# Optimization experiments

Hardware: AMD Instinct MI355X
Metric: run time of the kernel (lower is better)

Reference implementation:

```python
import jax, jax.numpy as jnp
import numpy as np

NUM_CLASSES = 2
THRESHOLD = 0.35
NEGPOS_RATIO = 7
VARIANCES = (0.1, 0.2)
B, P, O = 64, 16800, 64  # batch, num_priors, num_objs per image


def point_form(pr):
    # cxcywh -> xyxy
    return jnp.concatenate([pr[:, :2] - pr[:, 2:] / 2, pr[:, :2] + pr[:, 2:] / 2], axis=1)


def jaccard(a, b):
    # a: [A,4] xyxy, b: [Bx,4] xyxy -> IoU [A,Bx]
    lt = jnp.maximum(a[:, None, :2], b[None, :, :2])
    rb = jnp.minimum(a[:, None, 2:], b[None, :, 2:])
    wh = jnp.clip(rb - lt, 0.0)
    inter = wh[..., 0] * wh[..., 1]
    area_a = ((a[:, 2] - a[:, 0]) * (a[:, 3] - a[:, 1]))[:, None]
    area_b = ((b[:, 2] - b[:, 0]) * (b[:, 3] - b[:, 1]))[None, :]
    return inter / (area_a + area_b - inter)


def encode(matched, priors):
    # matched xyxy [P,4], priors cxcywh [P,4]
    g_cxcy = (matched[:, :2] + matched[:, 2:]) / 2 - priors[:, :2]
    g_cxcy = g_cxcy / (VARIANCES[0] * priors[:, 2:])
    g_wh = (matched[:, 2:] - matched[:, :2]) / priors[:, 2:]
    g_wh = jnp.log(g_wh) / VARIANCES[1]
    return jnp.concatenate([g_cxcy, g_wh], axis=1)


def encode_landm(matched, priors):
    # matched [P,10] -> [P,5,2]
    m = matched.reshape(-1, 5, 2)
    g = (m - priors[:, None, :2]) / (VARIANCES[0] * priors[:, None, 2:])
    return g.reshape(-1, 10)


def match_one(truths, labels, landms, priors):
    # truths [O,4], labels [O], landms [O,10]
    overlaps = jaccard(truths, point_form(priors))  # [O,P]
    best_prior_overlap = overlaps.max(axis=1)       # per-gt best IoU
    best_prior_idx = overlaps.argmax(axis=1)
    valid_gt = best_prior_overlap >= 0.2
    best_truth_overlap = overlaps.max(axis=0)       # per-prior best IoU
    best_truth_idx = overlaps.argmax(axis=0)
    # index_fill(2) only for valid gts (best_prior_idx_filter)
    bto = best_truth_overlap.at[best_prior_idx].set(
        jnp.where(valid_gt, 2.0, best_truth_overlap[best_prior_idx]))
    # ensure every gt keeps its best prior
    bti = best_truth_idx.at[best_prior_idx].set(jnp.arange(truths.shape[0]))
    matches = truths[bti]                  # [P,4]
    conf = labels[bti]                     # [P]
    conf = jnp.where(bto < THRESHOLD, 0.0, conf)
    loc = encode(matches, priors)
    landm = encode_landm(landms[bti], priors)
    return loc, conf, landm


def smooth_l1_sum(x, mask):
    ax = jnp.abs(x)
    v = jnp.where(ax < 1.0, 0.5 * ax * ax, ax - 0.5)
    return (v * mask).sum()


def setup_inputs() -> dict:
    key = jax.random.key(0)
    k1, k2, k3, k4, k5, k6, k7, k8 = jax.random.split(key, 8)
    loc_data = jax.random.normal(k1, (B, P, 4), jnp.float32)
    conf_data = jax.random.normal(k2, (B, P, NUM_CLASSES), jnp.float32)
    landm_data = jax.random.normal(k3, (B, P, 10), jnp.float32)
    # priors: cx,cy in (0,1), w,h in (0.02,0.22)
    cxy = jax.random.uniform(k4, (P, 2), jnp.float32)
    wh = jax.random.uniform(k5, (P, 2), jnp.float32) * 0.2 + 0.02
    priors = jnp.concatenate([cxy, wh], axis=1)
    # targets: valid corner boxes + landmarks + label in {1,-1}
    xy1 = jax.random.uniform(k6, (B, O, 2), jnp.float32) * 0.6
    bwh = jax.random.uniform(k7, (B, O, 2), jnp.float32) * 0.3 + 0.05
    boxes = jnp.concatenate([xy1, xy1 + bwh], axis=-1)
    lms = jax.random.uniform(k8, (B, O, 10), jnp.float32)
    lab = jnp.where(jax.random.uniform(jax.random.fold_in(key, 9), (B, O, 1)) < 0.3, -1.0, 1.0)
    targets = jnp.concatenate([boxes, lms, lab], axis=-1)
    return {"loc_data": loc_data, "conf_data": conf_data, "landm_data": landm_data,
            "priors": priors, "targets": targets}


def reference(loc_data, conf_data, landm_data, priors, targets):
    num = loc_data.shape[0]
    num_priors = priors.shape[0]
    truths = targets[:, :, :4]
    landms = targets[:, :, 4:14]
    labels = targets[:, :, -1]
    loc_t, conf_t, landm_t = jax.vmap(match_one, in_axes=(0, 0, 0, None))(
        truths, labels, landms, priors)  # [B,P,4], [B,P], [B,P,10]

    # landmark loss over conf_t > 0
    pos1 = conf_t > 0
    num_pos_landm = pos1.astype(jnp.int32).sum(axis=1, keepdims=True)
    N1 = jnp.maximum(num_pos_landm.sum().astype(jnp.float32), 1.0)
    loss_landm = smooth_l1_sum(landm_data - landm_t, pos1[..., None].astype(landm_data.dtype))

    # localization loss over conf_t != 0 ; conf_t[pos] = 1
    pos = conf_t != 0
    conf_t01 = jnp.where(pos, 1, 0)  # int {0,1}
    loss_l = smooth_l1_sum(loc_data - loc_t, pos[..., None].astype(loc_data.dtype))

    # hard negative mining on per-prior CE loss (global-max log_sum_exp, as in source)
    batch_conf = conf_data.reshape(-1, NUM_CLASSES)
    x_max = batch_conf.max()
    lse = jnp.log(jnp.exp(batch_conf - x_max).sum(axis=1, keepdims=True)) + x_max
    gathered = jnp.take_along_axis(batch_conf, conf_t01.reshape(-1, 1), axis=1)
    loss_c = (lse - gathered).reshape(num, -1)  # [B,P]; positives NOT zeroed (as in source)
    loss_idx = jnp.argsort(-loss_c, axis=1)
    idx_rank = jnp.argsort(loss_idx, axis=1)
    num_pos = pos.astype(jnp.int32).sum(axis=1, keepdims=True)  # [B,1]
    num_neg = jnp.minimum(NEGPOS_RATIO * num_pos, num_priors - 1)
    neg = idx_rank < num_neg  # [B,P]
    neg_pos = pos | neg

    # cross-entropy (sum) over selected pos+neg priors
    logp = jax.nn.log_softmax(conf_data, axis=-1)  # [B,P,C]
    ce = -jnp.take_along_axis(logp, conf_t01[..., None], axis=-1)[..., 0]
    loss_c_final = (ce * neg_pos.astype(ce.dtype)).sum()

    N = jnp.maximum(num_pos.sum().astype(jnp.float32), 1.0)
    return (loss_l / N, loss_c_final / N, loss_landm / N1)
```

## Files before the change

### kernel.cpp

```cpp
#include <hip/hip_runtime.h>
#include <math.h>

#define BN 64
#define PN 16800
#define ON 64
#define THRESH 0.35f
#define NEGPOS 7
#define GX 66
#define NBLK (BN * GX)
#define GXB 17
#define NBT (BN * GXB)
#define PT 4
#define TG 4
#define PSPLIT 2
#define PHALF 8400
#define NBP2 (BN * 16 * PSPLIT)
#define NBINS 4096
#define MAXM 4096
#define TAILT 104

struct GAcc {
  unsigned ticket;
  float sl, slm, sc;
  int np, np1;
  unsigned pad0, pad1;
};

__device__ __forceinline__ unsigned f2key(float f) {
  unsigned u = __float_as_uint(f);
  return (u & 0x80000000u) ? ~u : (u | 0x80000000u);
}
__device__ __forceinline__ float key2f(unsigned k) {
  unsigned u = (k & 0x80000000u) ? (k & 0x7FFFFFFFu) : ~k;
  return __uint_as_float(u);
}
__device__ __forceinline__ float sl1(float d) {
  float a = fabsf(d);
  return (a < 1.f) ? 0.5f * a * a : a - 0.5f;
}

__global__ void k_match2(const float* __restrict__ priors,
                         const float* __restrict__ targets,
                         float* __restrict__ bto, int* __restrict__ bti,
                         unsigned long long* __restrict__ bpp,
                         GAcc* __restrict__ gacc) {
  int bid = blockIdx.x;
  int tid = threadIdx.x;

  if (bid < NBT) {
    int b = bid / GXB;
    int slab = bid - b * GXB;
    int base = slab * 1024 + tid;
    if (bid == 0 && tid < 8) ((unsigned*)gacc)[tid] = 0;

    __shared__ float4 tbox[ON];
    __shared__ float tarea[ON];
    if (tid < ON) {
      const float* tg = &targets[((long)b * ON + tid) * 15];
      float4 bx = make_float4(tg[0], tg[1], tg[2], tg[3]);
      tbox[tid] = bx;
      tarea[tid] = (bx.z - bx.x) * (bx.w - bx.y);
    }
    __syncthreads();

    float px1[PT], py1[PT], px2[PT], py2[PT], ab[PT];
    bool val[PT];
#pragma unroll
    for (int i = 0; i < PT; i++) {
      int p = base + 256 * i;
      val[i] = p < PN;
      float4 pr = reinterpret_cast<const float4*>(priors)[val[i] ? p : base];
      px1[i] = pr.x - pr.z * 0.5f; py1[i] = pr.y - pr.w * 0.5f;
      px2[i] = pr.x + pr.z * 0.5f; py2[i] = pr.y + pr.w * 0.5f;
      ab[i] = (px2[i] - px1[i]) * (py2[i] - py1[i]);
    }
    float bi[PT], bu[PT]; int id[PT];
#pragma unroll
    for (int i = 0; i < PT; i++) { bi[i] = -1.f; bu[i] = 1.f; id[i] = 0; }

#pragma unroll 4
    for (int t = 0; t < ON; t++) {
      float4 a = tbox[t];
      float aa = tarea[t];
#pragma unroll
      for (int i = 0; i < PT; i++) {
        float lx = fmaxf(a.x, px1[i]), ly = fmaxf(a.y, py1[i]);
        float rx = fminf(a.z, px2[i]), ry = fminf(a.w, py2[i]);
        float w = fmaxf(rx - lx, 0.f), h = fmaxf(ry - ly, 0.f);
        float inter = w * h;
        float uni = aa + ab[i] - inter;
        if (inter * bu[i] > bi[i] * uni) { bi[i] = inter; bu[i] = uni; id[i] = t; }
      }
    }
#pragma unroll
    for (int i = 0; i < PT; i++) {
      if (val[i]) {
        int p = base + 256 * i;
        bto[(long)b * PN + p] = bi[i] / bu[i];
        bti[(long)b * PN + p] = id[i];
      }
    }
  } else {
    int id2 = bid - NBT;
    int b = id2 >> 5;
    int rest = id2 & 31;
    int g = rest >> 1;
    int h = rest & 1;
    int t0 = g * TG;
    float ax1[TG], ay1[TG], ax2[TG], ay2[TG], area_a[TG];
#pragma unroll
    for (int i = 0; i < TG; i++) {
      const float* tg = &targets[((long)b * ON + t0 + i) * 15];
      ax1[i] = tg[0]; ay1[i] = tg[1]; ax2[i] = tg[2]; ay2[i] = tg[3];
      area_a[i] = (ax2[i] - ax1[i]) * (ay2[i] - ay1[i]);
    }
    float bi[TG], bu[TG]; int bp[TG];
#pragma unroll
    for (int i = 0; i < TG; i++) { bi[i] = -1.f; bu[i] = 1.f; bp[i] = 0x7FFFFFFF; }
    int pend = (h + 1) * PHALF;
    for (int p = h * PHALF + tid; p < pend; p += 256) {
      float4 pr = reinterpret_cast<const float4*>(priors)[p];
      float px1 = pr.x - pr.z * 0.5f, py1 = pr.y - pr.w * 0.5f;
      float px2 = pr.x + pr.z * 0.5f, py2 = pr.y + pr.w * 0.5f;
      float area_b = (px2 - px1) * (py2 - py1);
#pragma unroll
      for (int i = 0; i < TG; i++) {
        float lx = fmaxf(ax1[i], px1), ly = fmaxf(ay1[i], py1);
        float rx = fminf(ax2[i], px2), ry = fminf(ay2[i], py2);
        float w = fmaxf(rx - lx, 0.f), h2 = fmaxf(ry - ly, 0.f);
        float inter = w * h2;
        float uni = area_a[i] + area_b - inter;
        if (inter * bu[i] > bi[i] * uni) { bi[i] = inter; bu[i] = uni; bp[i] = p; }
      }
    }
#pragma unroll
    for (int off = 1; off < 64; off <<= 1) {
#pragma unroll
      for (int i = 0; i < TG; i++) {
        float oi = __shfl_xor(bi[i], off), ou = __shfl_xor(bu[i], off);
        int op = __shfl_xor(bp[i], off);
        float a = oi * bu[i], c = bi[i] * ou;
        if (a > c || (a == c && op < bp[i])) { bi[i] = oi; bu[i] = ou; bp[i] = op; }
      }
    }
    __shared__ float si[TG][4], su[TG][4];
    __shared__ int spx[TG][4];
    int w = tid >> 6;
    if ((tid & 63) == 0) {
#pragma unroll
      for (int i = 0; i < TG; i++) { si[i][w] = bi[i]; su[i][w] = bu[i]; spx[i][w] = bp[i]; }
    }
    __syncthreads();
    if (tid < TG) {
      float fi = si[tid][0], fu = su[tid][0]; int fp = spx[tid][0];
      for (int ww = 1; ww < 4; ww++) {
        float a = si[tid][ww] * fu, c = fi * su[tid][ww];
        if (a > c || (a == c && spx[tid][ww] < fp)) { fi = si[tid][ww]; fu = su[tid][ww]; fp = spx[tid][ww]; }
      }
      float q = fi / fu;
      unsigned long long key = ((unsigned long long)f2key(q) << 32) | (unsigned)(~fp);
      bpp[((long)b * ON + t0 + tid) * PSPLIT + h] = key;
    }
  }
}

__global__ void k_encode(const float* __restrict__ loc_data,
                         const float* __restrict__ conf_data,
                         const float* __restrict__ landm_data,
                         const float* __restrict__ priors,
                         const float* __restrict__ targets,
                         const float* __restrict__ bto, const int* __restrict__ bti,
                         const unsigned long long* __restrict__ bpp,
                         float* __restrict__ lossc, unsigned char* __restrict__ posf,
                         float* __restrict__ part_l, float* __restrict__ part_lm,
                         int* __restrict__ np_part, int* __restrict__ np1_part) {
  int b = blockIdx.y;
  int p = blockIdx.x * 256 + threadIdx.x;
  int bid = b * GX + blockIdx.x;
  __shared__ float4 tgs4[ON * 15 / 4];
  __shared__ int ovr[256];
  float* tgs = (float*)tgs4;
  if (threadIdx.x < ON * 15 / 4)
    tgs4[threadIdx.x] = reinterpret_cast<const float4*>(targets + (long)b * ON * 15)[threadIdx.x];
  ovr[threadIdx.x] = -1;
  __syncthreads();
  if (threadIdx.x < ON) {
    int t = threadIdx.x;
    unsigned long long v0 = bpp[((long)b * ON + t) * PSPLIT];
    unsigned long long v1 = bpp[((long)b * ON + t) * PSPLIT + 1];
    unsigned long long best = v0 > v1 ? v0 : v1;
    float q = key2f((unsigned)(best >> 32));
    int qp = (int)(~(unsigned)best);
    int s0 = blockIdx.x * 256;
    if (qp >= s0 && qp < s0 + 256) {
      int valid = (q >= 0.2f) ? 1 : 0;
      atomicMax(&ovr[qp - s0], (t << 1) | valid);
    }
  }
  __syncthreads();

  float sum_l = 0.f, sum_lm = 0.f;
  int cp = 0, cp1 = 0;
  if (p < PN) {
    int t = bti[b * PN + p];
    float ov = bto[b * PN + p];
    int o = ovr[threadIdx.x];
    if (o >= 0) { t = o >> 1; if (o & 1) ov = 2.0f; }
    const float* tg = &tgs[t * 15];
    float label = tg[14];
    bool pos = ov >= THRESH;
    bool pos1 = pos && (label > 0.f);
    float4 pr = reinterpret_cast<const float4*>(priors)[p];
    if (pos) {
      float rz = 1.0f / pr.z, rw = 1.0f / pr.w;
      float m0 = tg[0], m1 = tg[1], m2 = tg[2], m3 = tg[3];
      float g0 = ((m0 + m2) * 0.5f - pr.x) * rz * 10.f;
      float g1 = ((m1 + m3) * 0.5f - pr.y) * rw * 10.f;
      float g2 = __logf((m2 - m0) * rz) * 5.f;
      float g3 = __logf((m3 - m1) * rw) * 5.f;
      const float* ld = &loc_data[((long)b * PN + p) * 4];
      sum_l = sl1(ld[0] - g0) + sl1(ld[1] - g1) + sl1(ld[2] - g2) + sl1(ld[3] - g3);
      cp = 1;
      if (pos1) {
        const float* lm = &landm_data[((long)b * PN + p) * 10];
#pragma unroll
        for (int i = 0; i < 5; i++) {
          float gx = (tg[4 + 2 * i] - pr.x) * rz * 10.f;
          float gy = (tg[5 + 2 * i] - pr.y) * rw * 10.f;
          sum_lm += sl1(lm[2 * i] - gx) + sl1(lm[2 * i + 1] - gy);
        }
        cp1 = 1;
      }
    }
    float2 c2 = reinterpret_cast<const float2*>(conf_data)[(long)b * PN + p];
    float m = fmaxf(c2.x, c2.y);
    float lse = m + __logf(__expf(c2.x - m) + __expf(c2.y - m));
    lossc[b * PN + p] = lse - (pos ? c2.y : c2.x);
    posf[b * PN + p] = pos ? 1 : 0;
  }
  for (int off = 32; off; off >>= 1) {
    sum_l += __shfl_down(sum_l, off);
    sum_lm += __shfl_down(sum_lm, off);
    cp += __shfl_down(cp, off);
    cp1 += __shfl_down(cp1, off);
  }
  __shared__ float sl4[4], slm4[4];
  __shared__ int sp4[4], sp14[4];
  int w = threadIdx.x >> 6;
  if ((threadIdx.x & 63) == 0) { sl4[w] = sum_l; slm4[w] = sum_lm; sp4[w] = cp; sp14[w] = cp1; }
  __syncthreads();
  if (threadIdx.x == 0) {
    part_l[bid] = sl4[0] + sl4[1] + sl4[2] + sl4[3];
    part_lm[bid] = slm4[0] + slm4[1] + slm4[2] + slm4[3];
    np_part[bid] = sp4[0] + sp4[1] + sp4[2] + sp4[3];
    np1_part[bid] = sp14[0] + sp14[1] + sp14[2] + sp14[3];
  }
}

__global__ void __launch_bounds__(1024) k_select(const float* __restrict__ lossc,
                                                 const unsigned char* __restrict__ posf,
                                                 const int* __restrict__ np_part,
                                                 const int* __restrict__ np1_part,
                                                 const float* __restrict__ part_l,
                                                 const float* __restrict__ part_lm,
                                                 GAcc* __restrict__ gacc,
                                                 float* __restrict__ out) {
  int b = blockIdx.x;
  int tid = threadIdx.x;
  int lane = tid & 63;
  int wv = tid >> 6;
  __shared__ unsigned hist[NBINS];
  __shared__ unsigned wtot[16];
  __shared__ float resv[MAXM];
  __shared__ int residx[MAXM];
  __shared__ int s_np, s_B, s_kp;
  __shared__ unsigned s_mc;
  const float* row = &lossc[(long)b * PN];
  const unsigned char* prow = &posf[(long)b * PN];

  if (tid == 0) s_np = 0;
  for (int i = tid; i < NBINS; i += 1024) hist[i] = 0;
  __syncthreads();
  if (tid < GX) atomicAdd(&s_np, np_part[b * GX + tid]);

  const float4* rf4 = reinterpret_cast<const float4*>(row);
  const uint4* pw4 = reinterpret_cast<const uint4*>(prow);
  bool hasTail = tid < TAILT;
  float vm[16];
  float vt[4];
  {
    float4 L0 = rf4[tid * 4], L1 = rf4[tid * 4 + 1], L2 = rf4[tid * 4 + 2], L3 = rf4[tid * 4 + 3];
    vm[0] = L0.x; vm[1] = L0.y; vm[2] = L0.z; vm[3] = L0.w;
    vm[4] = L1.x; vm[5] = L1.y; vm[6] = L1.z; vm[7] = L1.w;
    vm[8] = L2.x; vm[9] = L2.y; vm[10] = L2.z; vm[11] = L2.w;
    vm[12] = L3.x; vm[13] = L3.y; vm[14] = L3.z; vm[15] = L3.w;
  }
  unsigned pmask = 0;
  {
    uint4 W = pw4[tid];
    unsigned w0 = W.x, w1 = W.y, w2 = W.z, w3 = W.w;
#pragma unroll
    for (int j = 0; j < 4; j++) {
      pmask |= ((w0 >> (8 * j)) & 1u) << j;
      pmask |= ((w1 >> (8 * j)) & 1u) << (4 + j);
      pmask |= ((w2 >> (8 * j)) & 1u) << (8 + j);
      pmask |= ((w3 >> (8 * j)) & 1u) << (12 + j);
    }
  }
  unsigned tmask = 0;
  if (hasTail) {
    float4 Lt = rf4[4096 + tid];
    vt[0] = Lt.x; vt[1] = Lt.y; vt[2] = Lt.z; vt[3] = Lt.w;
    unsigned Wt = reinterpret_cast<const unsigned*>(prow)[4096 + tid];
#pragma unroll
    for (int j = 0; j < 4; j++) tmask |= ((Wt >> (8 * j)) & 1u) << j;
  } else {
    vt[0] = vt[1] = vt[2] = vt[3] = -1.f;
  }
  int bm[16], bt4[4];
#pragma unroll
  for (int j = 0; j < 16; j++) {
    int q = (int)(vm[j] * 256.0f);
    bm[j] = q < 0 ? 0 : (q > NBINS - 1 ? NBINS - 1 : q);
  }
#pragma unroll
  for (int j = 0; j < 4; j++) {
    int q = (int)(vt[j] * 256.0f);
    bt4[j] = q < 0 ? 0 : (q > NBINS - 1 ? NBINS - 1 : q);
  }
  __syncthreads();
  int np = s_np;
  int k = NEGPOS * np;
  if (k > PN - 1) k = PN - 1;
  bool haveNeg = (k > 0);

  int B = NBINS, kp = 0, m = 0;
  bool allB = false, fallback = false;
  if (haveNeg) {
#pragma unroll
    for (int j = 0; j < 16; j++) atomicAdd(&hist[bm[j]], 1u);
    if (hasTail) {
#pragma unroll
      for (int j = 0; j < 4; j++) atomicAdd(&hist[bt4[j]], 1u);
    }
    __syncthreads();
    int t4 = tid * 4;
    unsigned h0 = hist[t4], h1 = hist[t4 + 1], h2 = hist[t4 + 2], h3 = hist[t4 + 3];
    unsigned th = h0 + h1 + h2 + h3;
    unsigned v = th;
#pragma unroll
    for (int off = 1; off < 64; off <<= 1) {
      unsigned tv = (unsigned)__shfl_down((int)v, off);
      if (lane + off < 64) v += tv;
    }
    if (lane == 0) wtot[wv] = v;
    __syncthreads();
    unsigned add = 0;
    for (int w2 = wv + 1; w2 < 16; w2++) add += wtot[w2];
    unsigned S_t = v + add;
    unsigned S_next = S_t - th;
    if (S_t >= (unsigned)k && S_next < (unsigned)k) {
      unsigned run = S_next; int Bl; unsigned kpl;
      if (run + h3 >= (unsigned)k) { Bl = t4 + 3; kpl = k - run; }
      else { run += h3;
        if (run + h2 >= (unsigned)k) { Bl = t4 + 2; kpl = k - run; }
        else { run += h2;
          if (run + h1 >= (unsigned)k) { Bl = t4 + 1; kpl = k - run; }
          else { run += h1; Bl = t4; kpl = k - run; } } }
      s_B = Bl; s_kp = (int)kpl;
    }
    __syncthreads();
    B = s_B; kp = s_kp; m = (int)hist[B];
    allB = (kp == m);
    fallback = (!allB && m > MAXM);
  }

  float acc = 0.f;
  if (haveNeg && !allB && !fallback) {
    if (tid == 0) s_mc = 0;
    __syncthreads();
#pragma unroll
    for (int j = 0; j < 16; j++) {
      if (bm[j] == B) {
        unsigned slot = atomicAdd(&s_mc, 1u);
        resv[slot] = vm[j];
        residx[slot] = (tid * 16 + j) | (((pmask >> j) & 1u) ? 0x40000000 : 0);
      }
    }
    if (hasTail) {
#pragma unroll
      for (int j = 0; j < 4; j++) {
        if (bt4[j] == B) {
          unsigned slot = atomicAdd(&s_mc, 1u);
          resv[slot] = vt[j];
          residx[slot] = (16384 + tid * 4 + j) | (((tmask >> j) & 1u) ? 0x40000000 : 0);
        }
      }
    }
    __syncthreads();
    for (int i = tid; i < m; i += 1024) {
      float vi = resv[i];
      int pk = residx[i];
      int ii = pk & 0x3FFFFFFF;
      bool posi = (pk & 0x40000000) != 0;
      int rank = 0;
      for (int j = 0; j < m; j++) {
        float vj = resv[j];
        int ij = residx[j] & 0x3FFFFFFF;
        rank += (vj > vi || (vj == vi && ij < ii)) ? 1 : 0;
      }
      if (rank < kp && !posi) acc += vi;
    }
  }

  unsigned T = 0, R = 0, C = 0;
  if (fallback) {
    __shared__ unsigned s_lo, s_hi, fcnt[16];
    if (tid == 0) { s_lo = 0u; s_hi = 0xFFFFFFFFu; }
    __syncthreads();
    for (int it = 0; it < 32; it++) {
      unsigned lo = s_lo, hi = s_hi;
      unsigned mid = lo + ((hi - lo) >> 1) + ((hi - lo) & 1u);
      unsigned c = 0;
#pragma unroll
      for (int j = 0; j < 16; j++) c += (f2key(vm[j]) >= mid) ? 1u : 0u;
      if (hasTail) {
#pragma unroll
        for (int j = 0; j < 4; j++) c += (f2key(vt[j]) >= mid) ? 1u : 0u;
      }
#pragma unroll
      for (int o = 32; o; o >>= 1) c += (unsigned)__shfl_down((int)c, o);
      if (lane == 0) fcnt[wv] = c;
      __syncthreads();
      if (tid == 0) {
        unsigned tot = 0;
        for (int i = 0; i < 16; i++) tot += fcnt[i];
        if (tot >= (unsigned)k) s_lo = mid; else s_hi = mid - 1;
      }
      __syncthreads();
      if (s_lo >= s_hi) break;
    }
    T = s_lo;
    unsigned cg = 0, ce = 0;
#pragma unroll
    for (int j = 0; j < 16; j++) {
      unsigned key = f2key(vm[j]);
      cg += (key > T) ? 1u : 0u;
      ce += (key == T) ? 1u : 0u;
    }
    if (hasTail) {
#pragma unroll
      for (int j = 0; j < 4; j++) {
        unsigned key = f2key(vt[j]);
        cg += (key > T) ? 1u : 0u;
        ce += (key == T) ? 1u : 0u;
      }
    }
#pragma unroll
    for (int o = 32; o; o >>= 1) {
      cg += (unsigned)__shfl_down((int)cg, o);
      ce += (unsigned)__shfl_down((int)ce, o);
    }
    if (lane == 0) { fcnt[wv] = cg; wtot[wv] = ce; }
    __syncthreads();
    if (tid == 0) {
      unsigned tg2 = 0, te = 0;
      for (int i = 0; i < 16; i++) { tg2 += fcnt[i]; te += wtot[i]; }
      fcnt[0] = tg2; wtot[0] = te;
    }
    __syncthreads();
    C = wtot[0];
    R = (unsigned)k - fcnt[0];
    if (C != R && tid < 64) {
      unsigned running = 0;
      for (int base2 = 0; base2 < PN; base2 += 64) {
        int p = base2 + tid;
        bool tie = false, pos = false;
        float v2 = 0.f;
        if (p < PN) { v2 = row[p]; tie = (f2key(v2) == T); pos = prow[p] != 0; }
        unsigned long long mm = __ballot(tie);
        if (tie) {
          unsigned rank = running + (unsigned)__popcll(mm & ((1ull << tid) - 1));
          if (rank < R && !pos) acc += v2;
        }
        running += (unsigned)__popcll(mm);
      }
    }
  }

  unsigned ptc = 0;
#pragma unroll
  for (int j = 0; j < 16; j++) {
    float v2 = vm[j];
    bool pos = (pmask >> j) & 1u;
    if (pos) acc += v2;
    else if (haveNeg) {
      if (!fallback) {
        if (bm[j] > B || (bm[j] == B && allB)) acc += v2;
      } else {
        if (f2key(v2) > T) acc += v2;
      }
    }
    if (fallback && pos && f2key(v2) == T) ptc++;
  }
  if (hasTail) {
#pragma unroll
    for (int j = 0; j < 4; j++) {
      float v2 = vt[j];
      bool pos = (tmask >> j) & 1u;
      if (pos) acc += v2;
      else if (haveNeg) {
        if (!fallback) {
          if (bt4[j] > B || (bt4[j] == B && allB)) acc += v2;
        } else {
          if (f2key(v2) > T) acc += v2;
        }
      }
      if (fallback && pos && f2key(v2) == T) ptc++;
    }
  }
  for (int o = 32; o; o >>= 1) {
    acc += __shfl_down(acc, o);
    ptc += __shfl_down(ptc, o);
  }
  __shared__ float wsum[16];
  __shared__ unsigned wpt[16];
  if (lane == 0) { wsum[wv] = acc; wpt[wv] = ptc; }
  __syncthreads();

  __shared__ float s_rsl, s_rslm;
  __shared__ int s_rnp1;
  if (tid == 0) { s_rsl = 0.f; s_rslm = 0.f; s_rnp1 = 0; }
  __syncthreads();
  if (tid < GX) {
    atomicAdd(&s_rsl, part_l[b * GX + tid]);
    atomicAdd(&s_rslm, part_lm[b * GX + tid]);
    atomicAdd(&s_rnp1, np1_part[b * GX + tid]);
  }
  __syncthreads();

  if (tid == 0) {
    float tot = 0.f; unsigned pt = 0;
    for (int i = 0; i < 16; i++) { tot += wsum[i]; pt += wpt[i]; }
    if (fallback && C == R) tot += (float)(C - pt) * key2f(T);
    atomicAdd(&gacc->sc, tot);
    atomicAdd(&gacc->sl, s_rsl);
    atomicAdd(&gacc->slm, s_rslm);
    atomicAdd(&gacc->np, np);
    atomicAdd(&gacc->np1, s_rnp1);
  }
  __threadfence();
  __shared__ int lastF;
  if (tid == 0) lastF = (atomicAdd(&gacc->ticket, 1u) == (unsigned)(BN - 1)) ? 1 : 0;
  __syncthreads();
  if (lastF && tid == 0) {
    __threadfence();
    float sl = atomicAdd(&gacc->sl, 0.f);
    float slm = atomicAdd(&gacc->slm, 0.f);
    float sc = atomicAdd(&gacc->sc, 0.f);
    int tnp = atomicAdd(&gacc->np, 0);
    int tnp1 = atomicAdd(&gacc->np1, 0);
    float N = fmaxf((float)tnp, 1.f);
    float N1 = fmaxf((float)tnp1, 1.f);
    out[0] = sl / N;
    out[1] = sc / N;
    out[2] = slm / N1;
  }
}

extern "C" void kernel_launch(void* const* d_in, const int* in_sizes, int n_in,
                              void* d_out, int out_size, void* d_ws, size_t ws_size,
                              hipStream_t stream) {
  const float* loc_data = (const float*)d_in[0];
  const float* conf_data = (const float*)d_in[1];
  const float* landm_data = (const float*)d_in[2];
  const float* priors = (const float*)d_in[3];
  const float* targets = (const float*)d_in[4];
  float* out = (float*)d_out;

  char* ws = (char*)d_ws;
  const size_t SZ = (size_t)BN * PN * 4;
  size_t off = 0;
  float* lossc = (float*)(ws + off); off += SZ;
  float* bto = (float*)(ws + off); off += SZ;
  int* bti = (int*)(ws + off); off += SZ;
  unsigned char* posf = (unsigned char*)(ws + off); off += (size_t)BN * PN;
  off = (off + 15) & ~(size_t)15;
  unsigned long long* bpp = (unsigned long long*)(ws + off);
  off += (size_t)BN * ON * PSPLIT * 8;
  float* part_l = (float*)(ws + off); off += NBLK * 4;
  float* part_lm = (float*)(ws + off); off += NBLK * 4;
  int* np_part = (int*)(ws + off); off += NBLK * 4;
  int* np1_part = (int*)(ws + off); off += NBLK * 4;
  GAcc* gacc = (GAcc*)(ws + off); off += sizeof(GAcc);

  dim3 gbp(GX, BN);

  k_match2<<<NBT + NBP2, 256, 0, stream>>>(priors, targets, bto, bti, bpp, gacc);
  k_encode<<<gbp, 256, 0, stream>>>(loc_data, conf_data, landm_data, priors, targets,
                                    bto, bti, bpp, lossc, posf,
                                    part_l, part_lm, np_part, np1_part);
  k_select<<<BN, 1024, 0, stream>>>(lossc, posf, np_part, np1_part, part_l, part_lm,
                                    gacc, out);
}
```

Measured before the change: 208.7 us.

## Fuse encode stage into per-image select kernel, keeping loss values in registers

Merges the per-prior encode/loss kernel into the 1024-thread per-image selection kernel. Each thread computes its 16+4 priors' conf loss and positive flags directly into registers, which removes the round trip of reloading lossc/posf and the partial-sum arrays. Forced-match overrides now go through a shared bitmap plus a linear scan over fixes. The trade-off is that the encode work, previously spread over 4224 blocks, now runs on only 64 blocks, so less parallelism is available for the memory-heavy loads.

Result: slower. 242.1 us (+16.0%).

```diff
diff --git a/kernel.cpp b/kernel.cpp
--- a/kernel.cpp
+++ b/kernel.cpp
@@ -6,8 +6,6 @@
 #define ON 64
 #define THRESH 0.35f
 #define NEGPOS 7
-#define GX 66
-#define NBLK (BN * GX)
 #define GXB 17
 #define NBT (BN * GXB)
 #define PT 4
@@ -18,6 +16,7 @@
 #define NBINS 4096
 #define MAXM 4096
 #define TAILT 104
+#define BMW 525
 
 struct GAcc {
   unsigned ticket;
@@ -164,159 +163,208 @@
   }
 }
 
-__global__ void k_encode(const float* __restrict__ loc_data,
-                         const float* __restrict__ conf_data,
-                         const float* __restrict__ landm_data,
-                         const float* __restrict__ priors,
-                         const float* __restrict__ targets,
-                         const float* __restrict__ bto, const int* __restrict__ bti,
-                         const unsigned long long* __restrict__ bpp,
-                         float* __restrict__ lossc, unsigned char* __restrict__ posf,
-                         float* __restrict__ part_l, float* __restrict__ part_lm,
-                         int* __restrict__ np_part, int* __restrict__ np1_part) {
-  int b = blockIdx.y;
-  int p = blockIdx.x * 256 + threadIdx.x;
-  int bid = b * GX + blockIdx.x;
+__global__ void __launch_bounds__(1024) k_megasel(const float* __restrict__ priors,
+                                                  const float* __restrict__ targets,
+                                                  const float* __restrict__ loc_data,
+                                                  const float* __restrict__ conf_data,
+                                                  const float* __restrict__ landm_data,
+                                                  const float* __restrict__ bto,
+                                                  const int* __restrict__ bti,
+                                                  const unsigned long long* __restrict__ bpp,
+                                                  float* __restrict__ lossc,
+                                                  unsigned char* __restrict__ posf,
+                                                  GAcc* __restrict__ gacc,
+                                                  float* __restrict__ out) {
+  int b = blockIdx.x;
+  int tid = threadIdx.x;
+  int lane = tid & 63;
+  int wv = tid >> 6;
   __shared__ float4 tgs4[ON * 15 / 4];
-  __shared__ int ovr[256];
+  __shared__ unsigned bitmap[BMW];
+  __shared__ int fixq[ON];
+  __shared__ int fixinfo[ON];
+  __shared__ unsigned hist[NBINS];
+  __shared__ unsigned wtot[16];
+  __shared__ float wsl[16], wslm[16];
+  __shared__ unsigned wnp[16], wnp1[16];
+  __shared__ float resv[MAXM];
+  __shared__ int residx[MAXM];
+  __shared__ int s_B, s_kp;
+  __shared__ unsigned s_mc;
   float* tgs = (float*)tgs4;
-  if (threadIdx.x < ON * 15 / 4)
-    tgs4[threadIdx.x] = reinterpret_cast<const float4*>(targets + (long)b * ON * 15)[threadIdx.x];
-  ovr[threadIdx.x] = -1;
+  const float* row = &lossc[(long)b * PN];
+  const unsigned char* prow = &posf[(long)b * PN];
+
+  for (int i = tid; i < NBINS; i += 1024) hist[i] = 0;
+  for (int i = tid; i < BMW; i += 1024) bitmap[i] = 0;
+  if (tid < ON * 15 / 4)
+    tgs4[tid] = reinterpret_cast<const float4*>(targets + (long)b * ON * 15)[tid];
   __syncthreads();
-  if (threadIdx.x < ON) {
-    int t = threadIdx.x;
+
+  if (tid < ON) {
+    int t = tid;
     unsigned long long v0 = bpp[((long)b * ON + t) * PSPLIT];
     unsigned long long v1 = bpp[((long)b * ON + t) * PSPLIT + 1];
     unsigned long long best = v0 > v1 ? v0 : v1;
     float q = key2f((unsigned)(best >> 32));
     int qp = (int)(~(unsigned)best);
-    int s0 = blockIdx.x * 256;
-    if (qp >= s0 && qp < s0 + 256) {
-      int valid = (q >= 0.2f) ? 1 : 0;
-      atomicMax(&ovr[qp - s0], (t << 1) | valid);
-    }
+    bool valid = q >= 0.2f;
+    bool dupLater = false;
+    for (int j = 0; j < 64; j++) {
+      int ij = __shfl(qp, j);
+      if (j > t && ij == qp) dupLater = true;
+    }
+    fixq[t] = dupLater ? -1 : qp;
+    fixinfo[t] = (t << 1) | (valid ? 1 : 0);
+    if (!dupLater) atomicOr(&bitmap[qp >> 5], 1u << (qp & 31));
   }
   __syncthreads();
 
+  const float4* bto4 = reinterpret_cast<const float4*>(bto + (long)b * PN);
+  const int4* bti4 = reinterpret_cast<const int4*>(bti + (long)b * PN);
+  const float4* cf4 = reinterpret_cast<const float4*>(conf_data + (long)b * PN * 2);
+  float4* lc4 = reinterpret_cast<float4*>(lossc + (long)b * PN);
+  bool hasTail = tid < TAILT;
+
+  float vm[16], vt[4];
+  unsigned pmask = 0, tmask = 0;
   float sum_l = 0.f, sum_lm = 0.f;
-  int cp = 0, cp1 = 0;
-  if (p < PN) {
-    int t = bti[b * PN + p];
-    float ov = bto[b * PN + p];
-    int o = ovr[threadIdx.x];
-    if (o >= 0) { t = o >> 1; if (o & 1) ov = 2.0f; }
-    const float* tg = &tgs[t * 15];
-    float label = tg[14];
-    bool pos = ov >= THRESH;
-    bool pos1 = pos && (label > 0.f);
-    float4 pr = reinterpret_cast<const float4*>(priors)[p];
-    if (pos) {
-      float rz = 1.0f / pr.z, rw = 1.0f / pr.w;
-      float m0 = tg[0], m1 = tg[1], m2 = tg[2], m3 = tg[3];
-      float g0 = ((m0 + m2) * 0.5f - pr.x) * rz * 10.f;
-      float g1 = ((m1 + m3) * 0.5f - pr.y) * rw * 10.f;
-      float g2 = __logf((m2 - m0) * rz) * 5.f;
-      float g3 = __logf((m3 - m1) * rw) * 5.f;
-      const float* ld = &loc_data[((long)b * PN + p) * 4];
-      sum_l = sl1(ld[0] - g0) + sl1(ld[1] - g1) + sl1(ld[2] - g2) + sl1(ld[3] - g3);
-      cp = 1;
-      if (pos1) {
-        const float* lm = &landm_data[((long)b * PN + p) * 10];
-#pragma unroll
-        for (int i = 0; i < 5; i++) {
-          float gx = (tg[4 + 2 * i] - pr.x) * rz * 10.f;
-          float gy = (tg[5 + 2 * i] - pr.y) * rw * 10.f;
-          sum_lm += sl1(lm[2 * i] - gx) + sl1(lm[2 * i + 1] - gy);
+  unsigned cp = 0, cp1 = 0;
+
+#pragma unroll
+  for (int g4 = 0; g4 < 4; g4++) {
+    float4 O = bto4[tid * 4 + g4];
+    int4 T = bti4[tid * 4 + g4];
+    float4 Ca = cf4[tid * 8 + 2 * g4], Cb = cf4[tid * 8 + 2 * g4 + 1];
+    float ox[4] = {O.x, O.y, O.z, O.w};
+    int tx[4] = {T.x, T.y, T.z, T.w};
+    float xa[4] = {Ca.x, Ca.z, Cb.x, Cb.z};
+    float xb[4] = {Ca.y, Ca.w, Cb.y, Cb.w};
+#pragma unroll
+    for (int jj = 0; jj < 4; jj++) {
+      int j = g4 * 4 + jj;
+      int p = tid * 16 + j;
+      int t = tx[jj];
+      float ov = ox[jj];
+      if ((bitmap[p >> 5] >> (p & 31)) & 1u) {
+        for (int s = 0; s < ON; s++)
+          if (fixq[s] == p) { int inf = fixinfo[s]; t = inf >> 1; if (inf & 1) ov = 2.0f; }
+      }
+      const float* tg = &tgs[t * 15];
+      bool pos = ov >= THRESH;
+      if (pos) {
+        long gp = (long)b * PN + p;
+        float4 pr = reinterpret_cast<const float4*>(priors)[p];
+        float rz = 1.0f / pr.z, rw = 1.0f / pr.w;
+        float m0 = tg[0], m1 = tg[1], m2 = tg[2], m3 = tg[3];
+        float g0 = ((m0 + m2) * 0.5f - pr.x) * rz * 10.f;
+        float g1 = ((m1 + m3) * 0.5f - pr.y) * rw * 10.f;
+        float g2 = __logf((m2 - m0) * rz) * 5.f;
+        float g3 = __logf((m3 - m1) * rw) * 5.f;
+        const float* ld = &loc_data[gp * 4];
+        sum_l += sl1(ld[0] - g0) + sl1(ld[1] - g1) + sl1(ld[2] - g2) + sl1(ld[3] - g3);
+        cp++;
+        if (tg[14] > 0.f) {
+          const float* lm = &landm_data[gp * 10];
+#pragma unroll
+          for (int i = 0; i < 5; i++) {
+            float gx = (tg[4 + 2 * i] - pr.x) * rz * 10.f;
+            float gy = (tg[5 + 2 * i] - pr.y) * rw * 10.f;
+            sum_lm += sl1(lm[2 * i] - gx) + sl1(lm[2 * i + 1] - gy);
+          }
+          cp1++;
         }
-        cp1 = 1;
-      }
-    }
-    float2 c2 = reinterpret_cast<const float2*>(conf_data)[(long)b * PN + p];
-    float m = fmaxf(c2.x, c2.y);
-    float lse = m + __logf(__expf(c2.x - m) + __expf(c2.y - m));
-    lossc[b * PN + p] = lse - (pos ? c2.y : c2.x);
-    posf[b * PN + p] = pos ? 1 : 0;
-  }
-  for (int off = 32; off; off >>= 1) {
-    sum_l += __shfl_down(sum_l, off);
-    sum_lm += __shfl_down(sum_lm, off);
-    cp += __shfl_down(cp, off);
-    cp1 += __shfl_down(cp1, off);
-  }
-  __shared__ float sl4[4], slm4[4];
-  __shared__ int sp4[4], sp14[4];
-  int w = threadIdx.x >> 6;
-  if ((threadIdx.x & 63) == 0) { sl4[w] = sum_l; slm4[w] = sum_lm; sp4[w] = cp; sp14[w] = cp1; }
-  __syncthreads();
-  if (threadIdx.x == 0) {
-    part_l[bid] = sl4[0] + sl4[1] + sl4[2] + sl4[3];
-    part_lm[bid] = slm4[0] + slm4[1] + slm4[2] + slm4[3];
-    np_part[bid] = sp4[0] + sp4[1] + sp4[2] + sp4[3];
-    np1_part[bid] = sp14[0] + sp14[1] + sp14[2] + sp14[3];
-  }
-}
-
-__global__ void __launch_bounds__(1024) k_select(const float* __restrict__ lossc,
-                                                 const unsigned char* __restrict__ posf,
-                                                 const int* __restrict__ np_part,
-                                                 const int* __restrict__ np1_part,
-                                                 const float* __restrict__ part_l,
-                                                 const float* __restrict__ part_lm,
-                                                 GAcc* __restrict__ gacc,
-                                                 float* __restrict__ out) {
-  int b = blockIdx.x;
-  int tid = threadIdx.x;
-  int lane = tid & 63;
-  int wv = tid >> 6;
-  __shared__ unsigned hist[NBINS];
-  __shared__ unsigned wtot[16];
-  __shared__ float resv[MAXM];
-  __shared__ int residx[MAXM];
-  __shared__ int s_np, s_B, s_kp;
-  __shared__ unsigned s_mc;
-  const float* row = &lossc[(long)b * PN];
-  const unsigned char* prow = &posf[(long)b * PN];
-
-  if (tid == 0) s_np = 0;
-  for (int i = tid; i < NBINS; i += 1024) hist[i] = 0;
-  __syncthreads();
-  if (tid < GX) atomicAdd(&s_np, np_part[b * GX + tid]);
-
-  const float4* rf4 = reinterpret_cast<const float4*>(row);
-  const uint4* pw4 = reinterpret_cast<const uint4*>(prow);
-  bool hasTail = tid < TAILT;
-  float vm[16];
-  float vt[4];
+      }
+      float x0 = xa[jj], x1 = xb[jj];
+      float mm = fmaxf(x0, x1);
+      float lse = mm + __logf(__expf(x0 - mm) + __expf(x1 - mm));
+      vm[j] = lse - (pos ? x1 : x0);
+      if (pos) pmask |= 1u << j;
+    }
+    lc4[tid * 4 + g4] = make_float4(vm[g4 * 4], vm[g4 * 4 + 1], vm[g4 * 4 + 2], vm[g4 * 4 + 3]);
+  }
   {
-    float4 L0 = rf4[tid * 4], L1 = rf4[tid * 4 + 1], L2 = rf4[tid * 4 + 2], L3 = rf4[tid * 4 + 3];
-    vm[0] = L0.x; vm[1] = L0.y; vm[2] = L0.z; vm[3] = L0.w;
-    vm[4] = L1.x; vm[5] = L1.y; vm[6] = L1.z; vm[7] = L1.w;
-    vm[8] = L2.x; vm[9] = L2.y; vm[10] = L2.z; vm[11] = L2.w;
-    vm[12] = L3.x; vm[13] = L3.y; vm[14] = L3.z; vm[15] = L3.w;
-  }
-  unsigned pmask = 0;
-  {
-    uint4 W = pw4[tid];
-    unsigned w0 = W.x, w1 = W.y, w2 = W.z, w3 = W.w;
-#pragma unroll
-    for (int j = 0; j < 4; j++) {
-      pmask |= ((w0 >> (8 * j)) & 1u) << j;
-      pmask |= ((w1 >> (8 * j)) & 1u) << (4 + j);
-      pmask |= ((w2 >> (8 * j)) & 1u) << (8 + j);
-      pmask |= ((w3 >> (8 * j)) & 1u) << (12 + j);
-    }
-  }
-  unsigned tmask = 0;
+    unsigned pw0 = ((pmask >> 0) & 1u) | (((pmask >> 1) & 1u) << 8) | (((pmask >> 2) & 1u) << 16) | (((pmask >> 3) & 1u) << 24);
+    unsigned pw1 = ((pmask >> 4) & 1u) | (((pmask >> 5) & 1u) << 8) | (((pmask >> 6) & 1u) << 16) | (((pmask >> 7) & 1u) << 24);
+    unsigned pw2 = ((pmask >> 8) & 1u) | (((pmask >> 9) & 1u) << 8) | (((pmask >> 10) & 1u) << 16) | (((pmask >> 11) & 1u) << 24);
+    unsigned pw3 = ((pmask >> 12) & 1u) | (((pmask >> 13) & 1u) << 8) | (((pmask >> 14) & 1u) << 16) | (((pmask >> 15) & 1u) << 24);
+    reinterpret_cast<uint4*>(posf + (long)b * PN)[tid] = make_uint4(pw0, pw1, pw2, pw3);
+  }
   if (hasTail) {
-    float4 Lt = rf4[4096 + tid];
-    vt[0] = Lt.x; vt[1] = Lt.y; vt[2] = Lt.z; vt[3] = Lt.w;
-    unsigned Wt = reinterpret_cast<const unsigned*>(prow)[4096 + tid];
-#pragma unroll
-    for (int j = 0; j < 4; j++) tmask |= ((Wt >> (8 * j)) & 1u) << j;
+    float4 Ot = bto4[4096 + tid];
+    int4 Tt = bti4[4096 + tid];
+    float4 Ca = cf4[8192 + tid * 2], Cb = cf4[8192 + tid * 2 + 1];
+    float ox[4] = {Ot.x, Ot.y, Ot.z, Ot.w};
+    int tx[4] = {Tt.x, Tt.y, Tt.z, Tt.w};
+    float xa[4] = {Ca.x, Ca.z, Cb.x, Cb.z};
+    float xb[4] = {Ca.y, Ca.w, Cb.y, Cb.w};
+#pragma unroll
+    for (int jj = 0; jj < 4; jj++) {
+      int p = 16384 + tid * 4 + jj;
+      int t = tx[jj];
+      float ov = ox[jj];
+      if ((bitmap[p >> 5] >> (p & 31)) & 1u) {
+        for (int s = 0; s < ON; s++)
+          if (fixq[s] == p) { int inf = fixinfo[s]; t = inf >> 1; if (inf & 1) ov = 2.0f; }
+      }
+      const float* tg = &tgs[t * 15];
+      bool pos = ov >= THRESH;
+      if (pos) {
+        long gp = (long)b * PN + p;
+        float4 pr = reinterpret_cast<const float4*>(priors)[p];
+        float rz = 1.0f / pr.z, rw = 1.0f / pr.w;
+        float m0 = tg[0], m1 = tg[1], m2 = tg[2], m3 = tg[3];
+        float g0 = ((m0 + m2) * 0.5f - pr.x) * rz * 10.f;
+        float g1 = ((m1 + m3) * 0.5f - pr.y) * rw * 10.f;
+        float g2 = __logf((m2 - m0) * rz) * 5.f;
+        float g3 = __logf((m3 - m1) * rw) * 5.f;
+        const float* ld = &loc_data[gp * 4];
+        sum_l += sl1(ld[0] - g0) + sl1(ld[1] - g1) + sl1(ld[2] - g2) + sl1(ld[3] - g3);
+        cp++;
+        if (tg[14] > 0.f) {
+          const float* lm = &landm_data[gp * 10];
+#pragma unroll
+          for (int i = 0; i < 5; i++) {
+            float gx = (tg[4 + 2 * i] - pr.x) * rz * 10.f;
+            float gy = (tg[5 + 2 * i] - pr.y) * rw * 10.f;
+            sum_lm += sl1(lm[2 * i] - gx) + sl1(lm[2 * i + 1] - gy);
+          }
+          cp1++;
+        }
+      }
+      float x0 = xa[jj], x1 = xb[jj];
+      float mm = fmaxf(x0, x1);
+      float lse = mm + __logf(__expf(x0 - mm) + __expf(x1 - mm));
+      vt[jj] = lse - (pos ? x1 : x0);
+      if (pos) tmask |= 1u << jj;
+    }
+    lc4[4096 + tid] = make_float4(vt[0], vt[1], vt[2], vt[3]);
+    unsigned tw = ((tmask >> 0) & 1u) | (((tmask >> 1) & 1u) << 8) | (((tmask >> 2) & 1u) << 16) | (((tmask >> 3) & 1u) << 24);
+    reinterpret_cast<unsigned*>(posf + (long)b * PN)[4096 + tid] = tw;
   } else {
     vt[0] = vt[1] = vt[2] = vt[3] = -1.f;
   }
+
+  {
+    float rsl = sum_l, rslm = sum_lm;
+    unsigned rnp = cp, rnp1 = cp1;
+#pragma unroll
+    for (int o = 32; o; o >>= 1) {
+      rsl += __shfl_down(rsl, o);
+      rslm += __shfl_down(rslm, o);
+      rnp += (unsigned)__shfl_down((int)rnp, o);
+      rnp1 += (unsigned)__shfl_down((int)rnp1, o);
+    }
+    if (lane == 0) { wsl[wv] = rsl; wslm[wv] = rslm; wnp[wv] = rnp; wnp1[wv] = rnp1; }
+  }
+  __syncthreads();
+  unsigned npTot = 0;
+  for (int i = 0; i < 16; i++) npTot += wnp[i];
+  int np = (int)npTot;
+  int k = NEGPOS * np;
+  if (k > PN - 1) k = PN - 1;
+  bool haveNeg = (k > 0);
+
   int bm[16], bt4[4];
 #pragma unroll
   for (int j = 0; j < 16; j++) {
@@ -328,11 +376,6 @@
     int q = (int)(vt[j] * 256.0f);
     bt4[j] = q < 0 ? 0 : (q > NBINS - 1 ? NBINS - 1 : q);
   }
-  __syncthreads();
-  int np = s_np;
-  int k = NEGPOS * np;
-  if (k > PN - 1) k = PN - 1;
-  bool haveNeg = (k > 0);
 
   int B = NBINS, kp = 0, m = 0;
   bool allB = false, fallback = false;
@@ -519,35 +562,31 @@
       if (fallback && pos && f2key(v2) == T) ptc++;
     }
   }
-  for (int o = 32; o; o >>= 1) {
-    acc += __shfl_down(acc, o);
-    ptc += __shfl_down(ptc, o);
+  {
+#pragma unroll
+    for (int o = 32; o; o >>= 1) {
+      acc += __shfl_down(acc, o);
+      ptc += (unsigned)__shfl_down((int)ptc, o);
+    }
   }
   __shared__ float wsum[16];
   __shared__ unsigned wpt[16];
   if (lane == 0) { wsum[wv] = acc; wpt[wv] = ptc; }
   __syncthreads();
 
-  __shared__ float s_rsl, s_rslm;
-  __shared__ int s_rnp1;
-  if (tid == 0) { s_rsl = 0.f; s_rslm = 0.f; s_rnp1 = 0; }
-  __syncthreads();
-  if (tid < GX) {
-    atomicAdd(&s_rsl, part_l[b * GX + tid]);
-    atomicAdd(&s_rslm, part_lm[b * GX + tid]);
-    atomicAdd(&s_rnp1, np1_part[b * GX + tid]);
-  }
-  __syncthreads();
-
   if (tid == 0) {
     float tot = 0.f; unsigned pt = 0;
-    for (int i = 0; i < 16; i++) { tot += wsum[i]; pt += wpt[i]; }
+    float tsl = 0.f, tslm = 0.f; unsigned tnp1 = 0;
+    for (int i = 0; i < 16; i++) {
+      tot += wsum[i]; pt += wpt[i];
+      tsl += wsl[i]; tslm += wslm[i]; tnp1 += wnp1[i];
+    }
     if (fallback && C == R) tot += (float)(C - pt) * key2f(T);
     atomicAdd(&gacc->sc, tot);
-    atomicAdd(&gacc->sl, s_rsl);
-    atomicAdd(&gacc->slm, s_rslm);
+    atomicAdd(&gacc->sl, tsl);
+    atomicAdd(&gacc->slm, tslm);
     atomicAdd(&gacc->np, np);
-    atomicAdd(&gacc->np1, s_rnp1);
+    atomicAdd(&gacc->np1, (int)tnp1);
   }
   __threadfence();
   __shared__ int lastF;
@@ -588,18 +627,9 @@
   off = (off + 15) & ~(size_t)15;
   unsigned long long* bpp = (unsigned long long*)(ws + off);
   off += (size_t)BN * ON * PSPLIT * 8;
-  float* part_l = (float*)(ws + off); off += NBLK * 4;
-  float* part_lm = (float*)(ws + off); off += NBLK * 4;
-  int* np_part = (int*)(ws + off); off += NBLK * 4;
-  int* np1_part = (int*)(ws + off); off += NBLK * 4;
   GAcc* gacc = (GAcc*)(ws + off); off += sizeof(GAcc);
 
-  dim3 gbp(GX, BN);
-
   k_match2<<<NBT + NBP2, 256, 0, stream>>>(priors, targets, bto, bti, bpp, gacc);
-  k_encode<<<gbp, 256, 0, stream>>>(loc_data, conf_data, landm_data, priors, targets,
-                                    bto, bti, bpp, lossc, posf,
-                                    part_l, part_lm, np_part, np1_part);
-  k_select<<<BN, 1024, 0, stream>>>(lossc, posf, np_part, np1_part, part_l, part_lm,
-                                    gacc, out);
+  k_megasel<<<BN, 1024, 0, stream>>>(priors, targets, loc_data, conf_data, landm_data,
+                                     bto, bti, bpp, lossc, posf, gacc, out);
 }
```
